# Kernel optimization log

Hardware: AMD Instinct MI355X
Metric: run time of the kernel (lower is better)

## Reference

```python
import jax, jax.numpy as jnp
import numpy as np

# E2M1 (FP4) value table: low 3 bits magnitude, bit 3 sign (indices 8..15 negative)
FP4_TABLE = jnp.array([0.0, 0.5, 1.0, 1.5, 2.0, 3.0, 4.0, 6.0,
                       0.0, -0.5, -1.0, -1.5, -2.0, -3.0, -4.0, -6.0], dtype=jnp.float32)
FP4_BLOCK = 32  # per-row 1x32 scale groups


def dequant_fp4(packed, scale):
    """packed: [E, O, I//2] uint8 (two e2m1 nibbles per byte, low nibble first),
    scale: [E, O, I//32] float32 (e8m0, i.e. powers of two). Returns [E, O, I] float32."""
    lo = (packed & 15).astype(jnp.int32)
    hi = ((packed >> 4) & 15).astype(jnp.int32)
    # interleave low, high nibbles along the input dim (matches torch stack(...,-1).flatten)
    vals = FP4_TABLE[jnp.stack([lo, hi], axis=-1)]  # [E, O, I//2, 2]
    w = vals.reshape(packed.shape[0], packed.shape[1], packed.shape[2] * 2)
    return w * jnp.repeat(scale, FP4_BLOCK, axis=-1)


def setup_inputs() -> dict:
    T, H, F, E, K = 2048, 2048, 1024, 16, 4
    key = jax.random.key(0)
    k = jax.random.split(key, 8)
    hidden_states = jax.random.normal(k[0], (T, H), dtype=jnp.float32)
    topk_weights = jax.nn.softmax(jax.random.normal(k[1], (T, K)), axis=-1)
    topk_ids = jax.random.randint(k[2], (T, K), 0, E, dtype=jnp.int32)
    # checkpoint-native packed FP4 expert weights + e8m0 (power-of-two) scales
    gate_up_weight = jax.random.randint(k[3], (E, 2 * F, H // 2), 0, 256, dtype=jnp.int32).astype(jnp.uint8)
    gate_up_scale = jnp.exp2(jax.random.randint(k[4], (E, 2 * F, H // 32), -8, -5).astype(jnp.float32))
    down_weight = jax.random.randint(k[5], (E, H, F // 2), 0, 256, dtype=jnp.int32).astype(jnp.uint8)
    down_scale = jnp.exp2(jax.random.randint(k[6], (E, H, F // 32), -8, -5).astype(jnp.float32))
    return {"hidden_states": hidden_states, "topk_weights": topk_weights, "topk_ids": topk_ids,
            "gate_up_weight": gate_up_weight, "gate_up_scale": gate_up_scale,
            "down_weight": down_weight, "down_scale": down_scale}


def reference(hidden_states, topk_weights, topk_ids, gate_up_weight, gate_up_scale, down_weight, down_scale):
    # 1. dequantize checkpoint-native FP4 experts to dense float weights
    w_gate_up = dequant_fp4(gate_up_weight, gate_up_scale)  # [E, 2F, H]
    w_down = dequant_fp4(down_weight, down_scale)           # [E, H, F]
    T = hidden_states.shape[0]
    E = w_gate_up.shape[0]
    # 2. scatter routing weights into a dense [T, E] combine matrix
    combine = jnp.zeros((T, E), dtype=hidden_states.dtype)
    combine = combine.at[jnp.arange(T)[:, None], topk_ids].add(topk_weights)
    # 3. grouped expert GEMM (exact dense dispatch over experts)
    gu = jnp.einsum('th,eoh->teo', hidden_states, w_gate_up)  # [T, E, 2F]
    gate, up = jnp.split(gu, 2, axis=-1)                       # gate = first ffn_dim rows
    act = jax.nn.silu(gate) * up                               # SwiGLU (swiglu_limit=0 -> no clamping)
    act = act * combine[:, :, None]                            # fold routing weights into activations
    return jnp.einsum('tef,ehf->th', act, w_down)              # [T, H]
```

## Files before the change

### kernel.cpp

```cpp
#include <hip/hip_runtime.h>
#include <stdint.h>

#define HD 2048
#define FD 1024
#define NE 16
#define NPAIR 8192
#define BM 256
#define MAXT 48
#define LDK 40

typedef short bf16x8 __attribute__((ext_vector_type(8)));
typedef float f32x4 __attribute__((ext_vector_type(4)));
typedef unsigned short u16;

static __device__ __forceinline__ u16 f2bf(float f) {
  uint32_t u = __float_as_uint(f);
  u += 0x7FFFu + ((u >> 16) & 1u);
  return (u16)(u >> 16);
}

struct DqTab { uint32_t hA, hB, lA, lB; };

static __device__ __forceinline__ DqTab make_tab(uint32_t sbits) {
  int n = (int)(sbits >> 23) - 127;
  int q = n >> 1;
  uint32_t r = (uint32_t)(n & 1);
  uint32_t mq = (uint32_t)(-q);
  uint32_t sub1 = mq * 0x01010100u;
  uint32_t subA = mq * 0x01010101u;
  DqTab t;
  t.hA = (r ? 0x40403F00u : 0x3F3F3F00u) - sub1;
  t.hB = (r ? 0x41414040u : 0x40404040u) - subA;
  t.lA = r ? 0x40008000u : 0xC0800000u;
  t.lB = r ? 0x4000C080u : 0xC0804000u;
  return t;
}

static __device__ __forceinline__ void dq8(uint32_t p, const DqTab& t, uint32_t* d) {
  uint32_t a = p & 0x0F0F0F0Fu;
  uint32_t b = (p >> 4) & 0x0F0F0F0Fu;
  uint32_t x0 = __builtin_amdgcn_perm(b, a, 0x05010400u);
  uint32_t x1 = __builtin_amdgcn_perm(b, a, 0x07030602u);
  uint32_t m0 = x0 & 0x07070707u;
  uint32_t m1 = x1 & 0x07070707u;
  uint32_t h0 = __builtin_amdgcn_perm(t.hB, t.hA, m0) | ((x0 & 0x08080808u) << 4);
  uint32_t h1 = __builtin_amdgcn_perm(t.hB, t.hA, m1) | ((x1 & 0x08080808u) << 4);
  uint32_t l0 = __builtin_amdgcn_perm(t.lB, t.lA, m0);
  uint32_t l1 = __builtin_amdgcn_perm(t.lB, t.lA, m1);
  d[0] = __builtin_amdgcn_perm(h0, l0, 0x05010400u);
  d[1] = __builtin_amdgcn_perm(h0, l0, 0x07030602u);
  d[2] = __builtin_amdgcn_perm(h1, l1, 0x05010400u);
  d[3] = __builtin_amdgcn_perm(h1, l1, 0x07030602u);
}

static __device__ __forceinline__ uint32_t pack4(int4 v) {
  return (uint32_t)(v.x & 0xFF) | ((uint32_t)(v.y & 0xFF) << 8) |
         ((uint32_t)(v.z & 0xFF) << 16) | ((uint32_t)v.w << 24);
}

__global__ void cast_kernel(const float* __restrict__ x, u16* __restrict__ xb) {
  int i = blockIdx.x * 256 + threadIdx.x;
  float4 v = ((const float4*)x)[i];
  ushort4 o;
  o.x = f2bf(v.x); o.y = f2bf(v.y); o.z = f2bf(v.z); o.w = f2bf(v.w);
  ((ushort4*)xb)[i] = o;
}

__global__ void zero_kernel(float4* __restrict__ out) {
  out[blockIdx.x * 256 + threadIdx.x] = float4{0.f, 0.f, 0.f, 0.f};
}

__global__ void route_kernel(const int* __restrict__ ids, const float* __restrict__ tw,
                             int* __restrict__ rows, float* __restrict__ rw,
                             int* __restrict__ te, int* __restrict__ pidx) {
  __shared__ int cnt[NE], base[NE], run[NE];
  int tid = threadIdx.x;
  if (tid < NE) { cnt[tid] = 0; run[tid] = 0; }
  __syncthreads();
  for (int i = tid; i < NPAIR; i += 256) atomicAdd(&cnt[ids[i]], 1);
  __syncthreads();
  if (tid == 0) {
    int cum = 0;
    for (int e = 0; e < NE; ++e) {
      base[e] = cum;
      int nt = (cnt[e] + BM - 1) >> 8;
      for (int j = 0; j < nt; ++j) te[(cum >> 8) + j] = e;
      cum += nt << 8;
    }
    for (int t = cum >> 8; t < MAXT; ++t) te[t] = -1;
  }
  __syncthreads();
  for (int i = tid; i < MAXT * BM; i += 256) {
    rows[i] = -1;
    rw[i] = 0.f;
    if (pidx) pidx[i] = -1;
  }
  __syncthreads();
  for (int i = tid; i < NPAIR; i += 256) {
    int e = ids[i];
    int p = base[e] + atomicAdd(&run[e], 1);
    rows[p] = i >> 2;
    rw[p] = tw[i];
    if (pidx) pidx[p] = i;
  }
}

__global__ __launch_bounds__(256, 2) void gemm1_kernel(
    const u16* __restrict__ xb, const int* __restrict__ gup32,
    const uint32_t* __restrict__ gus, const int* __restrict__ rows,
    const float* __restrict__ rw, const int* __restrict__ te,
    u16* __restrict__ act) {
  const int tile = blockIdx.y;
  const int e = te[tile];
  if (e < 0) return;
  const int f0 = blockIdx.x * 64;

  __shared__ u16 sA[2][BM * LDK];
  __shared__ u16 sBg[2][64 * LDK];
  __shared__ u16 sBu[2][64 * LDK];
  __shared__ int rows_s[BM];
  __shared__ float rw_s[BM];

  const int tid = threadIdx.x;
  rows_s[tid] = rows[tile * BM + tid];
  rw_s[tid] = rw[tile * BM + tid];
  __syncthreads();

  int arow = rows_s[tid];
  arow = arow < 0 ? 0 : arow;
  const u16* aptr = xb + (size_t)arow * HD;
  const int lofsA = tid * LDK;

  const int bn = (tid & 127) >> 1;
  const int isUp = tid >> 7;
  const int o = isUp * 1024 + f0 + bn;
  const int skh = tid & 1;
  const int* bptr = gup32 + (size_t)(e * 2048 + o) * (HD / 2) + skh * 8;
  const uint32_t* sptr = gus + (size_t)(e * 2048 + o) * (HD / 32);
  const int lofsB = bn * LDK + skh * 16;

  const int lane = tid & 63;
  const int w = tid >> 6;
  const int q = lane >> 4, c = lane & 15;

  f32x4 Cg[4][4], Cu[4][4];
#pragma unroll
  for (int s = 0; s < 4; ++s)
#pragma unroll
    for (int t2 = 0; t2 < 4; ++t2) {
      Cg[s][t2] = f32x4{0.f, 0.f, 0.f, 0.f};
      Cu[s][t2] = f32x4{0.f, 0.f, 0.f, 0.f};
    }

  {
    uint4 a0 = *(const uint4*)(aptr);
    uint4 a1 = *(const uint4*)(aptr + 8);
    uint4 a2 = *(const uint4*)(aptr + 16);
    uint4 a3 = *(const uint4*)(aptr + 24);
    int4 w0 = *(const int4*)(bptr);
    int4 w1 = *(const int4*)(bptr + 4);
    uint32_t sb = sptr[0];
    DqTab t = make_tab(sb);
    uint32_t d0[4], d1[4];
    dq8(pack4(w0), t, d0);
    dq8(pack4(w1), t, d1);
    u16* sAp = &sA[0][lofsA];
    *(uint4*)sAp = a0;
    *(uint4*)(sAp + 8) = a1;
    *(uint4*)(sAp + 16) = a2;
    *(uint4*)(sAp + 24) = a3;
    u16* sBp = (isUp ? sBu[0] : sBg[0]) + lofsB;
    *(uint4*)sBp = make_uint4(d0[0], d0[1], d0[2], d0[3]);
    *(uint4*)(sBp + 8) = make_uint4(d1[0], d1[1], d1[2], d1[3]);
  }

  for (int kk = 0; kk < HD / 32; ++kk) {
    const int p = kk & 1;
    __syncthreads();
    uint4 na0, na1, na2, na3;
    int4 nw0, nw1;
    uint32_t nsb;
    if (kk < HD / 32 - 1) {
      const int k2 = (kk + 1) * 32;
      na0 = *(const uint4*)(aptr + k2);
      na1 = *(const uint4*)(aptr + k2 + 8);
      na2 = *(const uint4*)(aptr + k2 + 16);
      na3 = *(const uint4*)(aptr + k2 + 24);
      nw0 = *(const int4*)(bptr + (k2 >> 1));
      nw1 = *(const int4*)(bptr + (k2 >> 1) + 4);
      nsb = sptr[k2 >> 5];
    }

    bf16x8 af[4], bg[4], bu[4];
#pragma unroll
    for (int s = 0; s < 4; ++s)
      af[s] = *(const bf16x8*)&sA[p][(w * 64 + s * 16 + c) * LDK + q * 8];
#pragma unroll
    for (int t2 = 0; t2 < 4; ++t2) {
      bg[t2] = *(const bf16x8*)&sBg[p][(t2 * 16 + c) * LDK + q * 8];
      bu[t2] = *(const bf16x8*)&sBu[p][(t2 * 16 + c) * LDK + q * 8];
    }
#pragma unroll
    for (int s = 0; s < 4; ++s)
#pragma unroll
      for (int t2 = 0; t2 < 4; ++t2) {
        Cg[s][t2] = __builtin_amdgcn_mfma_f32_16x16x32_bf16(af[s], bg[t2], Cg[s][t2], 0, 0, 0);
        Cu[s][t2] = __builtin_amdgcn_mfma_f32_16x16x32_bf16(af[s], bu[t2], Cu[s][t2], 0, 0, 0);
      }

    if (kk < HD / 32 - 1) {
      DqTab t = make_tab(nsb);
      uint32_t d0[4], d1[4];
      dq8(pack4(nw0), t, d0);
      dq8(pack4(nw1), t, d1);
      u16* sAp = &sA[p ^ 1][lofsA];
      *(uint4*)sAp = na0;
      *(uint4*)(sAp + 8) = na1;
      *(uint4*)(sAp + 16) = na2;
      *(uint4*)(sAp + 24) = na3;
      u16* sBp = (isUp ? sBu[p ^ 1] : sBg[p ^ 1]) + lofsB;
      *(uint4*)sBp = make_uint4(d0[0], d0[1], d0[2], d0[3]);
      *(uint4*)(sBp + 8) = make_uint4(d1[0], d1[1], d1[2], d1[3]);
    }
  }

#pragma unroll
  for (int s = 0; s < 4; ++s) {
    const int mlb = w * 64 + s * 16 + q * 4;
#pragma unroll
    for (int t2 = 0; t2 < 4; ++t2) {
      const int fg = f0 + t2 * 16 + c;
#pragma unroll
      for (int r = 0; r < 4; ++r) {
        const int ml = mlb + r;
        float g = Cg[s][t2][r];
        float u = Cu[s][t2][r];
        float aval = g / (1.f + __expf(-g)) * u * rw_s[ml];
        act[(size_t)(tile * BM + ml) * FD + fg] = f2bf(aval);
      }
    }
  }
}

__global__ __launch_bounds__(256, 2) void gemm2_kernel(
    const u16* __restrict__ act, const int* __restrict__ dwn32,
    const uint32_t* __restrict__ dsc, const int* __restrict__ rows,
    const int* __restrict__ pidx, const int* __restrict__ te,
    float* __restrict__ out, float* __restrict__ pout) {
  const int tile = blockIdx.y;
  const int e = te[tile];
  if (e < 0) return;
  const int h0 = blockIdx.x * 128;

  __shared__ u16 sA[2][BM * LDK];
  __shared__ u16 sB[2][128 * LDK];
  __shared__ int rows_s[BM];
  __shared__ int pidx_s[BM];

  const int tid = threadIdx.x;
  rows_s[tid] = rows[tile * BM + tid];
  pidx_s[tid] = pout ? pidx[tile * BM + tid] : -1;
  __syncthreads();

  const u16* aptr = act + (size_t)(tile * BM + tid) * FD;
  const int lofsA = tid * LDK;

  const int bn = tid >> 1;
  const int skh = tid & 1;
  const int* bptr = dwn32 + (size_t)(e * 2048 + h0 + bn) * (FD / 2) + skh * 8;
  const uint32_t* sptr = dsc + (size_t)(e * 2048 + h0 + bn) * (FD / 32);
  const int lofsB = bn * LDK + skh * 16;

  const int lane = tid & 63;
  const int w = tid >> 6;
  const int q = lane >> 4, c = lane & 15;

  f32x4 Cd[4][8];
#pragma unroll
  for (int s = 0; s < 4; ++s)
#pragma unroll
    for (int t2 = 0; t2 < 8; ++t2) Cd[s][t2] = f32x4{0.f, 0.f, 0.f, 0.f};

  {
    uint4 a0 = *(const uint4*)(aptr);
    uint4 a1 = *(const uint4*)(aptr + 8);
    uint4 a2 = *(const uint4*)(aptr + 16);
    uint4 a3 = *(const uint4*)(aptr + 24);
    int4 w0 = *(const int4*)(bptr);
    int4 w1 = *(const int4*)(bptr + 4);
    uint32_t sb = sptr[0];
    DqTab t = make_tab(sb);
    uint32_t d0[4], d1[4];
    dq8(pack4(w0), t, d0);
    dq8(pack4(w1), t, d1);
    u16* sAp = &sA[0][lofsA];
    *(uint4*)sAp = a0;
    *(uint4*)(sAp + 8) = a1;
    *(uint4*)(sAp + 16) = a2;
    *(uint4*)(sAp + 24) = a3;
    u16* sBp = sB[0] + lofsB;
    *(uint4*)sBp = make_uint4(d0[0], d0[1], d0[2], d0[3]);
    *(uint4*)(sBp + 8) = make_uint4(d1[0], d1[1], d1[2], d1[3]);
  }

  for (int kk = 0; kk < FD / 32; ++kk) {
    const int p = kk & 1;
    __syncthreads();
    uint4 na0, na1, na2, na3;
    int4 nw0, nw1;
    uint32_t nsb;
    if (kk < FD / 32 - 1) {
      const int k2 = (kk + 1) * 32;
      na0 = *(const uint4*)(aptr + k2);
      na1 = *(const uint4*)(aptr + k2 + 8);
      na2 = *(const uint4*)(aptr + k2 + 16);
      na3 = *(const uint4*)(aptr + k2 + 24);
      nw0 = *(const int4*)(bptr + (k2 >> 1));
      nw1 = *(const int4*)(bptr + (k2 >> 1) + 4);
      nsb = sptr[k2 >> 5];
    }

    bf16x8 af[4], bf_[8];
#pragma unroll
    for (int s = 0; s < 4; ++s)
      af[s] = *(const bf16x8*)&sA[p][(w * 64 + s * 16 + c) * LDK + q * 8];
#pragma unroll
    for (int t2 = 0; t2 < 8; ++t2)
      bf_[t2] = *(const bf16x8*)&sB[p][(t2 * 16 + c) * LDK + q * 8];
#pragma unroll
    for (int s = 0; s < 4; ++s)
#pragma unroll
      for (int t2 = 0; t2 < 8; ++t2)
        Cd[s][t2] = __builtin_amdgcn_mfma_f32_16x16x32_bf16(af[s], bf_[t2], Cd[s][t2], 0, 0, 0);

    if (kk < FD / 32 - 1) {
      DqTab t = make_tab(nsb);
      uint32_t d0[4], d1[4];
      dq8(pack4(nw0), t, d0);
      dq8(pack4(nw1), t, d1);
      u16* sAp = &sA[p ^ 1][lofsA];
      *(uint4*)sAp = na0;
      *(uint4*)(sAp + 8) = na1;
      *(uint4*)(sAp + 16) = na2;
      *(uint4*)(sAp + 24) = na3;
      u16* sBp = sB[p ^ 1] + lofsB;
      *(uint4*)sBp = make_uint4(d0[0], d0[1], d0[2], d0[3]);
      *(uint4*)(sBp + 8) = make_uint4(d1[0], d1[1], d1[2], d1[3]);
    }
  }

  if (pout) {
#pragma unroll
    for (int s = 0; s < 4; ++s) {
      const int mlb = w * 64 + s * 16 + q * 4;
#pragma unroll
      for (int t2 = 0; t2 < 8; ++t2) {
        const int hg = h0 + t2 * 16 + c;
#pragma unroll
        for (int r = 0; r < 4; ++r) {
          int prow = pidx_s[mlb + r];
          if (prow >= 0) pout[(size_t)prow * HD + hg] = Cd[s][t2][r];
        }
      }
    }
  } else {
#pragma unroll
    for (int s = 0; s < 4; ++s) {
      const int mlb = w * 64 + s * 16 + q * 4;
#pragma unroll
      for (int t2 = 0; t2 < 8; ++t2) {
        const int hg = h0 + t2 * 16 + c;
#pragma unroll
        for (int r = 0; r < 4; ++r) {
          int token = rows_s[mlb + r];
          if (token >= 0) atomicAdd(&out[(size_t)token * HD + hg], Cd[s][t2][r]);
        }
      }
    }
  }
}

__global__ void finalize_kernel(const float4* __restrict__ pout, float4* __restrict__ out) {
  int j = blockIdx.x * 256 + threadIdx.x;
  int token = j >> 9;
  int col = j & 511;
  const float4* p = pout + ((size_t)token * 4) * 512 + col;
  float4 a = p[0], b = p[512], c = p[1024], d = p[1536];
  out[j] = float4{a.x + b.x + c.x + d.x, a.y + b.y + c.y + d.y,
                  a.z + b.z + c.z + d.z, a.w + b.w + c.w + d.w};
}

extern "C" void kernel_launch(void* const* d_in, const int* in_sizes, int n_in,
                              void* d_out, int out_size, void* d_ws, size_t ws_size,
                              hipStream_t stream) {
  const float* hidden = (const float*)d_in[0];
  const float* tw = (const float*)d_in[1];
  const int* ids = (const int*)d_in[2];
  const int* gup32 = (const int*)d_in[3];
  const uint32_t* gus = (const uint32_t*)d_in[4];
  const int* dwn32 = (const int*)d_in[5];
  const uint32_t* dsc = (const uint32_t*)d_in[6];
  float* out = (float*)d_out;

  char* ws = (char*)d_ws;
  int* rows = (int*)(ws);
  float* rw = (float*)(ws + 49152);
  int* te = (int*)(ws + 98304);
  u16* xb = (u16*)(ws + 131072);
  u16* act = (u16*)(ws + 8519680);

  const size_t POUT_OFF = 33685504ULL;
  const size_t PIDX_OFF = POUT_OFF + (size_t)NPAIR * HD * 4;
  const size_t WS_NEED = PIDX_OFF + (size_t)MAXT * BM * 4;
  const bool big = ws_size >= WS_NEED;
  float* pout = big ? (float*)(ws + POUT_OFF) : nullptr;
  int* pidx = big ? (int*)(ws + PIDX_OFF) : nullptr;

  cast_kernel<<<dim3(4096), dim3(256), 0, stream>>>(hidden, xb);
  if (!big) zero_kernel<<<dim3(4096), dim3(256), 0, stream>>>((float4*)out);
  route_kernel<<<dim3(1), dim3(256), 0, stream>>>(ids, tw, rows, rw, te, pidx);
  gemm1_kernel<<<dim3(16, MAXT), dim3(256), 0, stream>>>(xb, gup32, gus, rows, rw, te, act);
  gemm2_kernel<<<dim3(16, MAXT), dim3(256), 0, stream>>>(act, dwn32, dsc, rows, pidx, te, out, pout);
  if (big) finalize_kernel<<<dim3(1024 * 1024 / 256), dim3(256), 0, stream>>>((const float4*)pout, (float4*)out);
}
```

Baseline: 577.0 us.

## Stage packed FP4 weights in LDS and dequantize per-fragment at MFMA time

Both grouped GEMMs now load packed FP4 weight bytes and scales for four K-steps at once into LDS in a padded layout. Each wave dequantizes its own B fragments directly from LDS just before the MFMAs, instead of dequantizing once into bf16 shared tiles. This cuts LDS footprint and makes global weight loads wider and more coalesced. The cost is redundant dequant work, since every wave repeats the perm/table work for the same B fragment, and the kernel now holds more registers for eight prefetched int4s.

```diff
diff --git a/kernel.cpp b/kernel.cpp
--- a/kernel.cpp
+++ b/kernel.cpp
@@ -58,6 +58,17 @@
          ((uint32_t)(v.z & 0xFF) << 16) | ((uint32_t)v.w << 24);
 }
 
+static __device__ __forceinline__ bf16x8 dqfrag(const uint32_t* pB, const uint32_t* pS,
+                                                int row, int kkloc, int q) {
+  uint32_t pb = pB[row * 17 + kkloc * 4 + q];
+  DqTab t = make_tab(pS[row * 4 + kkloc]);
+  uint32_t d[4];
+  dq8(pb, t, d);
+  union { uint32_t u[4]; bf16x8 v; } cv;
+  cv.u[0] = d[0]; cv.u[1] = d[1]; cv.u[2] = d[2]; cv.u[3] = d[3];
+  return cv.v;
+}
+
 __global__ void cast_kernel(const float* __restrict__ x, u16* __restrict__ xb) {
   int i = blockIdx.x * 256 + threadIdx.x;
   float4 v = ((const float4*)x)[i];
@@ -116,8 +127,8 @@
   const int f0 = blockIdx.x * 64;
 
   __shared__ u16 sA[2][BM * LDK];
-  __shared__ u16 sBg[2][64 * LDK];
-  __shared__ u16 sBu[2][64 * LDK];
+  __shared__ uint32_t sBp[2][128 * 17];
+  __shared__ uint32_t sSc[2][128 * 4];
   __shared__ int rows_s[BM];
   __shared__ float rw_s[BM];
 
@@ -131,13 +142,13 @@
   const u16* aptr = xb + (size_t)arow * HD;
   const int lofsA = tid * LDK;
 
-  const int bn = (tid & 127) >> 1;
-  const int isUp = tid >> 7;
-  const int o = isUp * 1024 + f0 + bn;
-  const int skh = tid & 1;
-  const int* bptr = gup32 + (size_t)(e * 2048 + o) * (HD / 2) + skh * 8;
-  const uint32_t* sptr = gus + (size_t)(e * 2048 + o) * (HD / 32);
-  const int lofsB = bn * LDK + skh * 16;
+  const int srow = tid >> 4;
+  const int sseg = tid & 15;
+  const int* gb = gup32 + (size_t)(e * 2048 + f0 + srow) * 1024 + sseg * 4;
+  const int trow = tid >> 1;
+  const int tpair = (tid & 1) * 2;
+  const int to = trow < 64 ? f0 + trow : 1024 + f0 + (trow - 64);
+  const uint32_t* scb = gus + (size_t)(e * 2048 + to) * 64 + tpair;
 
   const int lane = tid & 63;
   const int w = tid >> 6;
@@ -152,75 +163,82 @@
       Cu[s][t2] = f32x4{0.f, 0.f, 0.f, 0.f};
     }
 
+  int4 breg[8];
+  uint2 sreg;
+
   {
+#pragma unroll
+    for (int pp = 0; pp < 8; ++pp)
+      breg[pp] = *(const int4*)(gb + (pp < 4 ? 0 : 983040) + pp * 16384);
+    sreg = *(const uint2*)scb;
     uint4 a0 = *(const uint4*)(aptr);
     uint4 a1 = *(const uint4*)(aptr + 8);
     uint4 a2 = *(const uint4*)(aptr + 16);
     uint4 a3 = *(const uint4*)(aptr + 24);
-    int4 w0 = *(const int4*)(bptr);
-    int4 w1 = *(const int4*)(bptr + 4);
-    uint32_t sb = sptr[0];
-    DqTab t = make_tab(sb);
-    uint32_t d0[4], d1[4];
-    dq8(pack4(w0), t, d0);
-    dq8(pack4(w1), t, d1);
+#pragma unroll
+    for (int pp = 0; pp < 8; ++pp)
+      sBp[0][(srow + pp * 16) * 17 + sseg] = pack4(breg[pp]);
+    sSc[0][trow * 4 + tpair] = sreg.x;
+    sSc[0][trow * 4 + tpair + 1] = sreg.y;
     u16* sAp = &sA[0][lofsA];
     *(uint4*)sAp = a0;
     *(uint4*)(sAp + 8) = a1;
     *(uint4*)(sAp + 16) = a2;
     *(uint4*)(sAp + 24) = a3;
-    u16* sBp = (isUp ? sBu[0] : sBg[0]) + lofsB;
-    *(uint4*)sBp = make_uint4(d0[0], d0[1], d0[2], d0[3]);
-    *(uint4*)(sBp + 8) = make_uint4(d1[0], d1[1], d1[2], d1[3]);
-  }
-
-  for (int kk = 0; kk < HD / 32; ++kk) {
+  }
+
+  for (int kk = 0; kk < 64; ++kk) {
     const int p = kk & 1;
+    const int sb = (kk >> 2) & 1;
+    const int kkloc = kk & 3;
     __syncthreads();
+
     uint4 na0, na1, na2, na3;
-    int4 nw0, nw1;
-    uint32_t nsb;
-    if (kk < HD / 32 - 1) {
-      const int k2 = (kk + 1) * 32;
-      na0 = *(const uint4*)(aptr + k2);
-      na1 = *(const uint4*)(aptr + k2 + 8);
-      na2 = *(const uint4*)(aptr + k2 + 16);
-      na3 = *(const uint4*)(aptr + k2 + 24);
-      nw0 = *(const int4*)(bptr + (k2 >> 1));
-      nw1 = *(const int4*)(bptr + (k2 >> 1) + 4);
-      nsb = sptr[k2 >> 5];
-    }
-
-    bf16x8 af[4], bg[4], bu[4];
+    if (kk < 63) {
+      const u16* ap = aptr + (kk + 1) * 32;
+      na0 = *(const uint4*)(ap);
+      na1 = *(const uint4*)(ap + 8);
+      na2 = *(const uint4*)(ap + 16);
+      na3 = *(const uint4*)(ap + 24);
+    }
+    if (kkloc == 0 && kk + 4 < 64) {
+      const int boff = ((kk >> 2) + 1) * 64;
+#pragma unroll
+      for (int pp = 0; pp < 8; ++pp)
+        breg[pp] = *(const int4*)(gb + boff + (pp < 4 ? 0 : 983040) + pp * 16384);
+      sreg = *(const uint2*)(scb + ((kk >> 2) + 1) * 4);
+    }
+
+    bf16x8 af[4];
 #pragma unroll
     for (int s = 0; s < 4; ++s)
       af[s] = *(const bf16x8*)&sA[p][(w * 64 + s * 16 + c) * LDK + q * 8];
+
 #pragma unroll
     for (int t2 = 0; t2 < 4; ++t2) {
-      bg[t2] = *(const bf16x8*)&sBg[p][(t2 * 16 + c) * LDK + q * 8];
-      bu[t2] = *(const bf16x8*)&sBu[p][(t2 * 16 + c) * LDK + q * 8];
-    }
-#pragma unroll
-    for (int s = 0; s < 4; ++s)
-#pragma unroll
-      for (int t2 = 0; t2 < 4; ++t2) {
-        Cg[s][t2] = __builtin_amdgcn_mfma_f32_16x16x32_bf16(af[s], bg[t2], Cg[s][t2], 0, 0, 0);
-        Cu[s][t2] = __builtin_amdgcn_mfma_f32_16x16x32_bf16(af[s], bu[t2], Cu[s][t2], 0, 0, 0);
+      bf16x8 bg = dqfrag(sBp[sb], sSc[sb], t2 * 16 + c, kkloc, q);
+      bf16x8 bu = dqfrag(sBp[sb], sSc[sb], 64 + t2 * 16 + c, kkloc, q);
+#pragma unroll
+      for (int s = 0; s < 4; ++s) {
+        Cg[s][t2] = __builtin_amdgcn_mfma_f32_16x16x32_bf16(af[s], bg, Cg[s][t2], 0, 0, 0);
+        Cu[s][t2] = __builtin_amdgcn_mfma_f32_16x16x32_bf16(af[s], bu, Cu[s][t2], 0, 0, 0);
       }
-
-    if (kk < HD / 32 - 1) {
-      DqTab t = make_tab(nsb);
-      uint32_t d0[4], d1[4];
-      dq8(pack4(nw0), t, d0);
-      dq8(pack4(nw1), t, d1);
+    }
+
+    if (kk < 63) {
       u16* sAp = &sA[p ^ 1][lofsA];
       *(uint4*)sAp = na0;
       *(uint4*)(sAp + 8) = na1;
       *(uint4*)(sAp + 16) = na2;
       *(uint4*)(sAp + 24) = na3;
-      u16* sBp = (isUp ? sBu[p ^ 1] : sBg[p ^ 1]) + lofsB;
-      *(uint4*)sBp = make_uint4(d0[0], d0[1], d0[2], d0[3]);
-      *(uint4*)(sBp + 8) = make_uint4(d1[0], d1[1], d1[2], d1[3]);
+    }
+    if (kkloc == 3 && kk < 63) {
+      const int sbn = sb ^ 1;
+#pragma unroll
+      for (int pp = 0; pp < 8; ++pp)
+        sBp[sbn][(srow + pp * 16) * 17 + sseg] = pack4(breg[pp]);
+      sSc[sbn][trow * 4 + tpair] = sreg.x;
+      sSc[sbn][trow * 4 + tpair + 1] = sreg.y;
     }
   }
 
@@ -253,7 +271,8 @@
   const int h0 = blockIdx.x * 128;
 
   __shared__ u16 sA[2][BM * LDK];
-  __shared__ u16 sB[2][128 * LDK];
+  __shared__ uint32_t sBp[2][128 * 17];
+  __shared__ uint32_t sSc[2][128 * 4];
   __shared__ int rows_s[BM];
   __shared__ int pidx_s[BM];
 
@@ -265,11 +284,12 @@
   const u16* aptr = act + (size_t)(tile * BM + tid) * FD;
   const int lofsA = tid * LDK;
 
-  const int bn = tid >> 1;
-  const int skh = tid & 1;
-  const int* bptr = dwn32 + (size_t)(e * 2048 + h0 + bn) * (FD / 2) + skh * 8;
-  const uint32_t* sptr = dsc + (size_t)(e * 2048 + h0 + bn) * (FD / 32);
-  const int lofsB = bn * LDK + skh * 16;
+  const int srow = tid >> 4;
+  const int sseg = tid & 15;
+  const int* gb = dwn32 + (size_t)(e * 2048 + h0 + srow) * 512 + sseg * 4;
+  const int trow = tid >> 1;
+  const int tpair = (tid & 1) * 2;
+  const uint32_t* scb = dsc + (size_t)(e * 2048 + h0 + trow) * 32 + tpair;
 
   const int lane = tid & 63;
   const int w = tid >> 6;
@@ -281,71 +301,79 @@
 #pragma unroll
     for (int t2 = 0; t2 < 8; ++t2) Cd[s][t2] = f32x4{0.f, 0.f, 0.f, 0.f};
 
+  int4 breg[8];
+  uint2 sreg;
+
   {
+#pragma unroll
+    for (int pp = 0; pp < 8; ++pp)
+      breg[pp] = *(const int4*)(gb + pp * 8192);
+    sreg = *(const uint2*)scb;
     uint4 a0 = *(const uint4*)(aptr);
     uint4 a1 = *(const uint4*)(aptr + 8);
     uint4 a2 = *(const uint4*)(aptr + 16);
     uint4 a3 = *(const uint4*)(aptr + 24);
-    int4 w0 = *(const int4*)(bptr);
-    int4 w1 = *(const int4*)(bptr + 4);
-    uint32_t sb = sptr[0];
-    DqTab t = make_tab(sb);
-    uint32_t d0[4], d1[4];
-    dq8(pack4(w0), t, d0);
-    dq8(pack4(w1), t, d1);
+#pragma unroll
+    for (int pp = 0; pp < 8; ++pp)
+      sBp[0][(srow + pp * 16) * 17 + sseg] = pack4(breg[pp]);
+    sSc[0][trow * 4 + tpair] = sreg.x;
+    sSc[0][trow * 4 + tpair + 1] = sreg.y;
     u16* sAp = &sA[0][lofsA];
     *(uint4*)sAp = a0;
     *(uint4*)(sAp + 8) = a1;
     *(uint4*)(sAp + 16) = a2;
     *(uint4*)(sAp + 24) = a3;
-    u16* sBp = sB[0] + lofsB;
-    *(uint4*)sBp = make_uint4(d0[0], d0[1], d0[2], d0[3]);
-    *(uint4*)(sBp + 8) = make_uint4(d1[0], d1[1], d1[2], d1[3]);
-  }
-
-  for (int kk = 0; kk < FD / 32; ++kk) {
+  }
+
+  for (int kk = 0; kk < 32; ++kk) {
     const int p = kk & 1;
+    const int sb = (kk >> 2) & 1;
+    const int kkloc = kk & 3;
     __syncthreads();
+
     uint4 na0, na1, na2, na3;
-    int4 nw0, nw1;
-    uint32_t nsb;
-    if (kk < FD / 32 - 1) {
-      const int k2 = (kk + 1) * 32;
-      na0 = *(const uint4*)(aptr + k2);
-      na1 = *(const uint4*)(aptr + k2 + 8);
-      na2 = *(const uint4*)(aptr + k2 + 16);
-      na3 = *(const uint4*)(aptr + k2 + 24);
-      nw0 = *(const int4*)(bptr + (k2 >> 1));
-      nw1 = *(const int4*)(bptr + (k2 >> 1) + 4);
-      nsb = sptr[k2 >> 5];
-    }
-
-    bf16x8 af[4], bf_[8];
+    if (kk < 31) {
+      const u16* ap = aptr + (kk + 1) * 32;
+      na0 = *(const uint4*)(ap);
+      na1 = *(const uint4*)(ap + 8);
+      na2 = *(const uint4*)(ap + 16);
+      na3 = *(const uint4*)(ap + 24);
+    }
+    if (kkloc == 0 && kk + 4 < 32) {
+      const int boff = ((kk >> 2) + 1) * 64;
+#pragma unroll
+      for (int pp = 0; pp < 8; ++pp)
+        breg[pp] = *(const int4*)(gb + boff + pp * 8192);
+      sreg = *(const uint2*)(scb + ((kk >> 2) + 1) * 4);
+    }
+
+    bf16x8 af[4];
 #pragma unroll
     for (int s = 0; s < 4; ++s)
       af[s] = *(const bf16x8*)&sA[p][(w * 64 + s * 16 + c) * LDK + q * 8];
-#pragma unroll
-    for (int t2 = 0; t2 < 8; ++t2)
-      bf_[t2] = *(const bf16x8*)&sB[p][(t2 * 16 + c) * LDK + q * 8];
-#pragma unroll
-    for (int s = 0; s < 4; ++s)
-#pragma unroll
-      for (int t2 = 0; t2 < 8; ++t2)
-        Cd[s][t2] = __builtin_amdgcn_mfma_f32_16x16x32_bf16(af[s], bf_[t2], Cd[s][t2], 0, 0, 0);
-
-    if (kk < FD / 32 - 1) {
-      DqTab t = make_tab(nsb);
-      uint32_t d0[4], d1[4];
-      dq8(pack4(nw0), t, d0);
-      dq8(pack4(nw1), t, d1);
+
+#pragma unroll
+    for (int t2 = 0; t2 < 8; ++t2) {
+      bf16x8 bf_ = dqfrag(sBp[sb], sSc[sb], t2 * 16 + c, kkloc, q);
+#pragma unroll
+      for (int s = 0; s < 4; ++s)
+        Cd[s][t2] = __builtin_amdgcn_mfma_f32_16x16x32_bf16(af[s], bf_, Cd[s][t2], 0, 0, 0);
+    }
+
+    if (kk < 31) {
       u16* sAp = &sA[p ^ 1][lofsA];
       *(uint4*)sAp = na0;
       *(uint4*)(sAp + 8) = na1;
       *(uint4*)(sAp + 16) = na2;
       *(uint4*)(sAp + 24) = na3;
-      u16* sBp = sB[p ^ 1] + lofsB;
-      *(uint4*)sBp = make_uint4(d0[0], d0[1], d0[2], d0[3]);
-      *(uint4*)(sBp + 8) = make_uint4(d1[0], d1[1], d1[2], d1[3]);
+    }
+    if (kkloc == 3 && kk < 31) {
+      const int sbn = sb ^ 1;
+#pragma unroll
+      for (int pp = 0; pp < 8; ++pp)
+        sBp[sbn][(srow + pp * 16) * 17 + sseg] = pack4(breg[pp]);
+      sSc[sbn][trow * 4 + tpair] = sreg.x;
+      sSc[sbn][trow * 4 + tpair + 1] = sreg.y;
     }
   }
 
```

Measured after the change: 561.1 us. 2.8% less time.
